# Kernel tuning notes

Measured on AMD Instinct MI355X. Metric: run time of the kernel, lower is better.

Reference implementation:

```python
import jax, jax.numpy as jnp
import numpy as np

ALPHA = 0.2  # LeakyReLU negative slope


def _gat_layer(x, edge_src, edge_dst, edge_embed, a, a2, concat):
    # torch: edge_h = cat(input[edge[0]], input[edge[1]], edge_embed).t(); scatter rows = edge[0]
    h = jnp.concatenate([x[edge_src], x[edge_dst], edge_embed], axis=1)  # [E, 2F+R]
    edge_m = h @ a.T                                                      # [E, D]
    powers = -jax.nn.leaky_relu(edge_m @ a2, ALPHA)                       # [E]
    edge_e = jnp.exp(powers)                                              # [E]
    N = x.shape[0]
    rowsum = jax.ops.segment_sum(edge_e, edge_src, num_segments=N)        # [N]
    rowsum = jnp.where(rowsum == 0.0, 1e-12, rowsum)
    h_prime = jax.ops.segment_sum(edge_e[:, None] * edge_m, edge_src, num_segments=N)  # [N, D]
    h_prime = h_prime / rowsum[:, None]
    return jax.nn.elu(h_prime) if concat else h_prime


def _spgat_forward(entity_embeddings, relation_embed, edge_embed, a, a2, W,
                   a_out, a2_out, edge_list, edge_type, edge_list_nhop, edge_type_nhop):
    nheads = a.shape[0]
    # concatenate 1-hop and n-hop edges (as in torch forward of the attention layer)
    src = jnp.concatenate([edge_list[0], edge_list_nhop[0]], axis=0)
    dst = jnp.concatenate([edge_list[1], edge_list_nhop[1]], axis=0)
    ee_nhop = relation_embed[edge_type_nhop[:, 0]] + relation_embed[edge_type_nhop[:, 1]]
    ee_all = jnp.concatenate([edge_embed, ee_nhop], axis=0)               # [E+E2, R]
    heads = [_gat_layer(entity_embeddings, src, dst, ee_all, a[i], a2[i], True)
             for i in range(nheads)]
    x = jnp.concatenate(heads, axis=1)                                    # [N, H*F] (dropout = identity, eval)
    out_relation_1 = relation_embed @ W                                   # [n_rel, H*F]
    ee2 = out_relation_1[edge_type]
    ee2_nhop = out_relation_1[edge_type_nhop[:, 0]] + out_relation_1[edge_type_nhop[:, 1]]
    ee2_all = jnp.concatenate([ee2, ee2_nhop], axis=0)                    # [E+E2, H*F]
    x = jax.nn.elu(_gat_layer(x, src, dst, ee2_all, a_out, a2_out, False))
    return x, out_relation_1


def setup_inputs() -> dict:
    key = jax.random.key(0)
    N, F, R, NREL, E, E2, H = 50000, 128, 128, 500, 150000, 30000, 2
    ks = jax.random.split(key, 12)

    def xavier(k, shape):
        fan_in, fan_out = shape[-1], shape[-2]
        std = 1.414 * np.sqrt(2.0 / (fan_in + fan_out))
        return (jax.random.normal(k, shape, dtype=jnp.float32) * std).astype(jnp.float32)

    return {
        "entity_embeddings": jax.random.normal(ks[0], (N, F), dtype=jnp.float32),
        "relation_embed": jax.random.normal(ks[1], (NREL, R), dtype=jnp.float32),
        "edge_embed": jax.random.normal(ks[2], (E, R), dtype=jnp.float32),
        "edge_list": jax.random.randint(ks[3], (2, E), 0, N),
        "edge_type": jax.random.randint(ks[4], (E,), 0, NREL),
        "edge_list_nhop": jax.random.randint(ks[5], (2, E2), 0, N),
        "edge_type_nhop": jax.random.randint(ks[6], (E2, 2), 0, NREL),
        "a": xavier(ks[7], (H, F, 2 * F + R)),            # per-head a: [D, 2F+R]
        "a2": xavier(ks[8], (H, 1, F))[:, 0, :],          # per-head a_2: [D]
        "W": xavier(ks[9], (R, H * F)),
        "a_out": xavier(ks[10], (H * F, 3 * H * F)),      # out layer: in=H*F, nrela=H*F
        "a2_out": xavier(ks[11], (1, H * F))[0],
    }


def reference(entity_embeddings, relation_embed, edge_embed, edge_list, edge_type,
              edge_list_nhop, edge_type_nhop, a, a2, W, a_out, a2_out):
    return _spgat_forward(entity_embeddings, relation_embed, edge_embed, a, a2, W,
                          a_out, a2_out, edge_list, edge_type, edge_list_nhop, edge_type_nhop)
```

## Files before the change

### kernel.cpp

```cpp
#include <hip/hip_runtime.h>
#include <cstdint>
#include <cstddef>

#define N_NODES 50000
#define MP1     50048
#define NRELC   500
#define E1      150000
#define MP2     150016
#define E2N     30000
#define ETOT    180000
#define ALPHA_F 0.2f

typedef __attribute__((ext_vector_type(8))) short bf16x8;
typedef __attribute__((ext_vector_type(4))) float f32x4;

__device__ __forceinline__ float bf2f(unsigned short s) {
  return __uint_as_float((unsigned)s << 16);
}
__device__ __forceinline__ unsigned short f2bf(float f) {
  unsigned u = __float_as_uint(f);
  u += 0x7fff + ((u >> 16) & 1);
  return (unsigned short)(u >> 16);
}

__global__ void zero_int(int* __restrict__ p, int n) {
  int i = blockIdx.x * blockDim.x + threadIdx.x;
  if (i < n) p[i] = 0;
}

__global__ void build_edges(const int* __restrict__ el, const int* __restrict__ elnh,
                            int* __restrict__ src, int* __restrict__ dst) {
  int e = blockIdx.x * blockDim.x + threadIdx.x;
  if (e >= ETOT) return;
  if (e < E1) { src[e] = el[e];        dst[e] = el[E1 + e]; }
  else        { int k = e - E1; src[e] = elnh[k]; dst[e] = elnh[E2N + k]; }
}

__global__ void count_edges(const int* __restrict__ src, int* __restrict__ cnt) {
  int e = blockIdx.x * blockDim.x + threadIdx.x;
  if (e < ETOT) atomicAdd(&cnt[src[e]], 1);
}

__global__ void scan_counts(const int* __restrict__ cnt, int* __restrict__ rowptr) {
  __shared__ int lds[1024];
  __shared__ int carry;
  if (threadIdx.x == 0) carry = 0;
  __syncthreads();
  for (int base = 0; base < N_NODES; base += 1024) {
    int i = base + (int)threadIdx.x;
    int v = (i < N_NODES) ? cnt[i] : 0;
    lds[threadIdx.x] = v;
    __syncthreads();
    for (int off = 1; off < 1024; off <<= 1) {
      int t = (threadIdx.x >= (unsigned)off) ? lds[threadIdx.x - off] : 0;
      __syncthreads();
      lds[threadIdx.x] += t;
      __syncthreads();
    }
    int incl = lds[threadIdx.x];
    if (i < N_NODES) rowptr[i] = carry + incl - v;
    __syncthreads();
    if (threadIdx.x == 1023) carry += lds[1023];
    __syncthreads();
  }
  if (threadIdx.x == 0) rowptr[N_NODES] = carry;
}

__global__ void copy_int(const int* __restrict__ a, int* __restrict__ b, int n) {
  int i = blockIdx.x * blockDim.x + threadIdx.x;
  if (i < n) b[i] = a[i];
}

__global__ void fill_csr(const int* __restrict__ src, int* __restrict__ pos, int* __restrict__ csr) {
  int e = blockIdx.x * blockDim.x + threadIdx.x;
  if (e >= ETOT) return;
  int p = atomicAdd(&pos[src[e]], 1);
  csr[p] = e;
}

__global__ void pack_weea3(const float* __restrict__ a, float* __restrict__ o) {
  int i = blockIdx.x * blockDim.x + threadIdx.x;
  if (i >= 256 * 128) return;
  int c = i >> 7, k = i & 127;
  int h = c >> 7, d = c & 127;
  o[i] = a[h * 49152 + d * 384 + 256 + k];
}
__global__ void pack_wtw(const float* __restrict__ w, float* __restrict__ o) {
  int i = blockIdx.x * blockDim.x + threadIdx.x;
  if (i >= 256 * 128) return;
  int n = i >> 7, k = i & 127;
  o[i] = w[k * 256 + n];
}
__global__ void pack_wa3out(const float* __restrict__ ao, float* __restrict__ o) {
  int i = blockIdx.x * blockDim.x + threadIdx.x;
  if (i >= 256 * 256) return;
  int d = i >> 8, k = i & 255;
  o[i] = ao[d * 768 + 512 + k];
}
__global__ void pack_wxa_bf(const float* __restrict__ a, unsigned short* __restrict__ o) {
  int i = blockIdx.x * blockDim.x + threadIdx.x;
  if (i >= 512 * 128) return;
  int c = i >> 7, k = i & 127;
  int h = c >> 8, part = (c >> 7) & 1, d = c & 127;
  o[i] = f2bf(a[h * 49152 + d * 384 + part * 128 + k]);
}
__global__ void pack_weea3_bf(const float* __restrict__ a, unsigned short* __restrict__ o) {
  int i = blockIdx.x * blockDim.x + threadIdx.x;
  if (i >= 256 * 128) return;
  int c = i >> 7, k = i & 127;
  int h = c >> 7, d = c & 127;
  o[i] = f2bf(a[h * 49152 + d * 384 + 256 + k]);
}
__global__ void pack_wx1a_bf(const float* __restrict__ ao, unsigned short* __restrict__ o) {
  int i = blockIdx.x * blockDim.x + threadIdx.x;
  if (i >= 512 * 256) return;
  int c = i >> 8, k = i & 255;
  int part = c >> 8, d = c & 255;
  o[i] = f2bf(ao[d * 768 + part * 256 + k]);
}

__global__ __launch_bounds__(256) void gemm_bt_f32(
    const float* __restrict__ A, const float* __restrict__ Wt,
    float* __restrict__ C, int M, int N, int K) {
  __shared__ float As[32][132];
  __shared__ float Bs[32][132];
  const int bm = blockIdx.x * 128;
  const int bn = blockIdx.y * 128;
  const int tid = threadIdx.x;
  const int tx = tid & 15;
  const int ty = tid >> 4;
  float acc[8][8];
#pragma unroll
  for (int i = 0; i < 8; ++i)
#pragma unroll
    for (int j = 0; j < 8; ++j) acc[i][j] = 0.f;

  const int lr = tid >> 3;
  const int lc = (tid & 7) << 2;

  for (int k0 = 0; k0 < K; k0 += 32) {
#pragma unroll
    for (int i = 0; i < 4; ++i) {
      const int row = lr + (i << 5);
      float4 av = make_float4(0.f, 0.f, 0.f, 0.f);
      float4 bv = make_float4(0.f, 0.f, 0.f, 0.f);
      const int ga = bm + row, gb = bn + row;
      if (ga < M) av = *reinterpret_cast<const float4*>(A + (size_t)ga * K + k0 + lc);
      if (gb < N) bv = *reinterpret_cast<const float4*>(Wt + (size_t)gb * K + k0 + lc);
      As[lc + 0][row] = av.x; As[lc + 1][row] = av.y; As[lc + 2][row] = av.z; As[lc + 3][row] = av.w;
      Bs[lc + 0][row] = bv.x; Bs[lc + 1][row] = bv.y; Bs[lc + 2][row] = bv.z; Bs[lc + 3][row] = bv.w;
    }
    __syncthreads();
    for (int kk = 0; kk < 32; ++kk) {
      float a8[8], b8[8];
      *(float4*)&a8[0] = *(const float4*)&As[kk][ty * 8];
      *(float4*)&a8[4] = *(const float4*)&As[kk][ty * 8 + 4];
      *(float4*)&b8[0] = *(const float4*)&Bs[kk][tx * 8];
      *(float4*)&b8[4] = *(const float4*)&Bs[kk][tx * 8 + 4];
#pragma unroll
      for (int i = 0; i < 8; ++i)
#pragma unroll
        for (int j = 0; j < 8; ++j) acc[i][j] = fmaf(a8[i], b8[j], acc[i][j]);
    }
    __syncthreads();
  }
#pragma unroll
  for (int i = 0; i < 8; ++i) {
    const int gr = bm + ty * 8 + i;
    if (gr < M) {
      float4 v0 = make_float4(acc[i][0], acc[i][1], acc[i][2], acc[i][3]);
      float4 v1 = make_float4(acc[i][4], acc[i][5], acc[i][6], acc[i][7]);
      *reinterpret_cast<float4*>(C + (size_t)gr * N + bn + tx * 8) = v0;
      *reinterpret_cast<float4*>(C + (size_t)gr * N + bn + tx * 8 + 4) = v1;
    }
  }
}

template <typename TA, int K>
__global__ __launch_bounds__(256) void gemm_mfma(
    const TA* __restrict__ A, const unsigned short* __restrict__ Wt,
    unsigned short* __restrict__ C, int Mreal, int N) {
  __shared__ __align__(16) unsigned short lds[2][8192];
  const int tid  = threadIdx.x;
  const int wave = tid >> 6;
  const int lane = tid & 63;
  const int bm = blockIdx.x * 128;
  const int bn = blockIdx.y * 128;
  const int wr = wave >> 1, wc = wave & 1;
  constexpr int NT = K / 32;

  f32x4 acc[4][4] = {};

  const int rb   = lane & 15;
  const int cofs = ((lane >> 4) ^ (lane & 3)) << 3;

  auto stageB = [&](int buf, int kt) {
#pragma unroll
    for (int j = 0; j < 2; ++j) {
      const int o   = (wave * 2 + j) * 1024 + lane * 16;
      const int row = o >> 6;
      const int sc  = (o & 63) ^ ((row & 3) << 4);
      const char* g = (const char*)Wt + (size_t)(bn + row) * (K * 2) + kt * 64 + sc;
      __builtin_amdgcn_global_load_lds(
          (const __attribute__((address_space(1))) void*)g,
          (__attribute__((address_space(3))) void*)&lds[buf][4096 + (wave * 2 + j) * 512],
          16, 0, 0);
    }
  };
  auto stageA = [&](int buf, int kt) {
    if constexpr (sizeof(TA) == 2) {
#pragma unroll
      for (int j = 0; j < 2; ++j) {
        const int o   = (wave * 2 + j) * 1024 + lane * 16;
        const int row = o >> 6;
        const int sc  = (o & 63) ^ ((row & 3) << 4);
        const char* g = (const char*)A + (size_t)(bm + row) * (K * 2) + kt * 64 + sc;
        __builtin_amdgcn_global_load_lds(
            (const __attribute__((address_space(1))) void*)g,
            (__attribute__((address_space(3))) void*)&lds[buf][(wave * 2 + j) * 512],
            16, 0, 0);
      }
    } else {
#pragma unroll
      for (int p = 0; p < 2; ++p) {
        const int o   = p * 4096 + tid * 16;
        const int row = o >> 6;
        const int ke  = ((o & 63) ^ ((row & 3) << 4)) >> 1;
        const int gr  = bm + row;
        float v[8];
#pragma unroll
        for (int q = 0; q < 8; ++q) v[q] = 0.f;
        if (gr < Mreal) {
          const float* gp = (const float*)A + (size_t)gr * K + kt * 32 + ke;
          float4 u0 = *(const float4*)gp;
          float4 u1 = *(const float4*)(gp + 4);
          v[0] = u0.x; v[1] = u0.y; v[2] = u0.z; v[3] = u0.w;
          v[4] = u1.x; v[5] = u1.y; v[6] = u1.z; v[7] = u1.w;
        }
        bf16x8 pk;
#pragma unroll
        for (int q = 0; q < 8; ++q) pk[q] = (short)f2bf(v[q]);
        *(bf16x8*)&lds[buf][o >> 1] = pk;
      }
    }
  };

  stageA(0, 0); stageB(0, 0);
  for (int t = 0; t < NT; ++t) {
    __syncthreads();
    if (t + 1 < NT) { stageA((t + 1) & 1, t + 1); stageB((t + 1) & 1, t + 1); }
    const int buf = t & 1;
    bf16x8 af[4], bfr[4];
#pragma unroll
    for (int m = 0; m < 4; ++m)
      af[m] = *(const bf16x8*)&lds[buf][(rb + 16 * m + 64 * wr) * 32 + cofs];
#pragma unroll
    for (int n = 0; n < 4; ++n)
      bfr[n] = *(const bf16x8*)&lds[buf][4096 + (rb + 16 * n + 64 * wc) * 32 + cofs];
#pragma unroll
    for (int m = 0; m < 4; ++m)
#pragma unroll
      for (int n = 0; n < 4; ++n)
        acc[m][n] = __builtin_amdgcn_mfma_f32_16x16x32_bf16(af[m], bfr[n], acc[m][n], 0, 0, 0);
  }

  const int ccol = bn + wc * 64 + rb;
  const int crow = bm + wr * 64 + ((lane >> 4) << 2);
#pragma unroll
  for (int m = 0; m < 4; ++m)
#pragma unroll
    for (int n = 0; n < 4; ++n)
#pragma unroll
      for (int r = 0; r < 4; ++r)
        C[(size_t)(crow + 16 * m + r) * N + ccol + 16 * n] = f2bf(acc[m][n][r]);
}

__global__ __launch_bounds__(256) void agg1(
    const unsigned short* __restrict__ xa, const unsigned short* __restrict__ eeA31,
    const float* __restrict__ relA3, const int* __restrict__ rowptr,
    const int* __restrict__ csr, const int* __restrict__ dst,
    const int* __restrict__ etnh, const float* __restrict__ a2,
    unsigned short* __restrict__ x1) {
  int w = blockIdx.x * 4 + (threadIdx.x >> 6);
  int n = w >> 1, h = w & 1;
  if (n >= N_NODES) return;
  int l = threadIdx.x & 63;
  float w2a = a2[h * 128 + l];
  float w2b = a2[h * 128 + 64 + l];
  const unsigned short* xan = xa + (size_t)n * 512 + h * 256;
  float s0 = bf2f(xan[l]), s1 = bf2f(xan[64 + l]);
  float acc0 = 0.f, acc1 = 0.f, rs = 0.f;
  int p0 = rowptr[n], p1 = rowptr[n + 1];
  for (int p = p0; p < p1; ++p) {
    int e = csr[p];
    int d = dst[e];
    const unsigned short* xad = xa + (size_t)d * 512 + h * 256 + 128;
    float m0 = s0 + bf2f(xad[l]);
    float m1 = s1 + bf2f(xad[64 + l]);
    if (e < E1) {
      const unsigned short* ee = eeA31 + (size_t)e * 256 + h * 128;
      m0 += bf2f(ee[l]); m1 += bf2f(ee[64 + l]);
    } else {
      int k = e - E1;
      int t0 = etnh[2 * k], t1 = etnh[2 * k + 1];
      const float* r0 = relA3 + t0 * 256 + h * 128;
      const float* r1 = relA3 + t1 * 256 + h * 128;
      m0 += r0[l] + r1[l];
      m1 += r0[64 + l] + r1[64 + l];
    }
    float dot = m0 * w2a + m1 * w2b;
#pragma unroll
    for (int off = 32; off; off >>= 1) dot += __shfl_xor(dot, off);
    float lk = dot > 0.f ? dot : ALPHA_F * dot;
    float ev = __expf(-lk);
    acc0 = fmaf(ev, m0, acc0);
    acc1 = fmaf(ev, m1, acc1);
    rs += ev;
  }
  if (rs == 0.f) rs = 1e-12f;
  float inv = 1.f / rs;
  float h0 = acc0 * inv, h1 = acc1 * inv;
  h0 = h0 > 0.f ? h0 : (__expf(h0) - 1.f);
  h1 = h1 > 0.f ? h1 : (__expf(h1) - 1.f);
  x1[(size_t)n * 256 + h * 128 + l] = f2bf(h0);
  x1[(size_t)n * 256 + h * 128 + 64 + l] = f2bf(h1);
}

__global__ __launch_bounds__(256) void agg2(
    const unsigned short* __restrict__ x1a, const float* __restrict__ rel2,
    const int* __restrict__ rowptr, const int* __restrict__ csr,
    const int* __restrict__ dst, const int* __restrict__ etype,
    const int* __restrict__ etnh, const float* __restrict__ a2o,
    float* __restrict__ out) {
  int n = blockIdx.x * 4 + (threadIdx.x >> 6);
  if (n >= N_NODES) return;
  int l = threadIdx.x & 63;
  float w2[4], s[4], acc[4] = {0.f, 0.f, 0.f, 0.f};
#pragma unroll
  for (int j = 0; j < 4; ++j) {
    w2[j] = a2o[j * 64 + l];
    s[j] = bf2f(x1a[(size_t)n * 512 + j * 64 + l]);
  }
  float rs = 0.f;
  int p0 = rowptr[n], p1 = rowptr[n + 1];
  for (int p = p0; p < p1; ++p) {
    int e = csr[p];
    int d = dst[e];
    const unsigned short* xd = x1a + (size_t)d * 512 + 256;
    float m[4];
    if (e < E1) {
      int t = etype[e];
      const float* r = rel2 + t * 256;
#pragma unroll
      for (int j = 0; j < 4; ++j) m[j] = s[j] + bf2f(xd[j * 64 + l]) + r[j * 64 + l];
    } else {
      int k = e - E1;
      int t0 = etnh[2 * k], t1 = etnh[2 * k + 1];
      const float* r0 = rel2 + t0 * 256;
      const float* r1 = rel2 + t1 * 256;
#pragma unroll
      for (int j = 0; j < 4; ++j) m[j] = s[j] + bf2f(xd[j * 64 + l]) + r0[j * 64 + l] + r1[j * 64 + l];
    }
    float dot = 0.f;
#pragma unroll
    for (int j = 0; j < 4; ++j) dot = fmaf(m[j], w2[j], dot);
#pragma unroll
    for (int off = 32; off; off >>= 1) dot += __shfl_xor(dot, off);
    float lk = dot > 0.f ? dot : ALPHA_F * dot;
    float ev = __expf(-lk);
#pragma unroll
    for (int j = 0; j < 4; ++j) acc[j] = fmaf(ev, m[j], acc[j]);
    rs += ev;
  }
  if (rs == 0.f) rs = 1e-12f;
  float inv = 1.f / rs;
#pragma unroll
  for (int j = 0; j < 4; ++j) {
    float hv = acc[j] * inv;
    hv = hv > 0.f ? hv : (__expf(hv) - 1.f);
    out[(size_t)n * 256 + j * 64 + l] = hv;
  }
}

extern "C" void kernel_launch(void* const* d_in, const int* in_sizes, int n_in,
                              void* d_out, int out_size, void* d_ws, size_t ws_size,
                              hipStream_t stream) {
  const float* x    = (const float*)d_in[0];
  const float* rel  = (const float*)d_in[1];
  const float* eemb = (const float*)d_in[2];
  const int*   el   = (const int*)d_in[3];
  const int*   et   = (const int*)d_in[4];
  const int*   elnh = (const int*)d_in[5];
  const int*   etnh = (const int*)d_in[6];
  const float* a    = (const float*)d_in[7];
  const float* a2   = (const float*)d_in[8];
  const float* W    = (const float*)d_in[9];
  const float* aout = (const float*)d_in[10];
  const float* a2o  = (const float*)d_in[11];

  char* ws = (char*)d_ws;
  size_t cur = 0;
  auto alloc = [&](size_t bytes) {
    size_t o = cur;
    cur = (cur + bytes + 511) & ~(size_t)511;
    return o;
  };
  int* src     = (int*)(ws + alloc((size_t)ETOT * 4));
  int* dstv    = (int*)(ws + alloc((size_t)ETOT * 4));
  int* rowptr  = (int*)(ws + alloc((size_t)(N_NODES + 1) * 4));
  int* pos     = (int*)(ws + alloc((size_t)N_NODES * 4));
  int* csr     = (int*)(ws + alloc((size_t)ETOT * 4));
  float* weea3f = (float*)(ws + alloc((size_t)256 * 128 * 4));
  float* wtw    = (float*)(ws + alloc((size_t)256 * 128 * 4));
  float* wa3o   = (float*)(ws + alloc((size_t)256 * 256 * 4));
  unsigned short* wxa_bf   = (unsigned short*)(ws + alloc((size_t)512 * 128 * 2));
  unsigned short* weea3_bf = (unsigned short*)(ws + alloc((size_t)256 * 128 * 2));
  unsigned short* wx1a_bf  = (unsigned short*)(ws + alloc((size_t)512 * 256 * 2));
  float* relA3 = (float*)(ws + alloc((size_t)NRELC * 256 * 4));
  float* rel2  = (float*)(ws + alloc((size_t)NRELC * 256 * 4));
  unsigned short* x1B = (unsigned short*)(ws + alloc((size_t)MP1 * 256 * 2));
  unsigned short* xaB = (unsigned short*)(ws + alloc((size_t)MP1 * 512 * 2));
  unsigned short* eeB = (unsigned short*)(ws + alloc((size_t)MP2 * 256 * 2));
  (void)ws_size; (void)in_sizes; (void)n_in; (void)out_size;

  float* out_x    = (float*)d_out;
  float* out_rel1 = out_x + (size_t)N_NODES * 256;

  zero_int<<<(N_NODES + 255) / 256, 256, 0, stream>>>(pos, N_NODES);
  build_edges<<<(ETOT + 255) / 256, 256, 0, stream>>>(el, elnh, src, dstv);
  count_edges<<<(ETOT + 255) / 256, 256, 0, stream>>>(src, pos);
  scan_counts<<<1, 1024, 0, stream>>>(pos, rowptr);
  copy_int<<<(N_NODES + 255) / 256, 256, 0, stream>>>(rowptr, pos, N_NODES);
  fill_csr<<<(ETOT + 255) / 256, 256, 0, stream>>>(src, pos, csr);

  pack_weea3<<<(256 * 128 + 255) / 256, 256, 0, stream>>>(a, weea3f);
  pack_wtw<<<(256 * 128 + 255) / 256, 256, 0, stream>>>(W, wtw);
  pack_wa3out<<<(256 * 256 + 255) / 256, 256, 0, stream>>>(aout, wa3o);
  pack_wxa_bf<<<(512 * 128 + 255) / 256, 256, 0, stream>>>(a, wxa_bf);
  pack_weea3_bf<<<(256 * 128 + 255) / 256, 256, 0, stream>>>(a, weea3_bf);
  pack_wx1a_bf<<<(512 * 256 + 255) / 256, 256, 0, stream>>>(aout, wx1a_bf);

  gemm_mfma<float, 128><<<dim3(MP1 / 128, 4), 256, 0, stream>>>(x, wxa_bf, xaB, N_NODES, 512);
  gemm_mfma<float, 128><<<dim3(MP2 / 128, 2), 256, 0, stream>>>(eemb, weea3_bf, eeB, E1, 256);
  gemm_bt_f32<<<dim3((NRELC + 127) / 128, 2), 256, 0, stream>>>(rel, weea3f, relA3, NRELC, 256, 128);

  agg1<<<(N_NODES * 2 + 3) / 4, 256, 0, stream>>>(xaB, eeB, relA3, rowptr, csr, dstv, etnh, a2, x1B);

  gemm_bt_f32<<<dim3((NRELC + 127) / 128, 2), 256, 0, stream>>>(rel, wtw, out_rel1, NRELC, 256, 128);
  gemm_bt_f32<<<dim3((NRELC + 127) / 128, 2), 256, 0, stream>>>(out_rel1, wa3o, rel2, NRELC, 256, 256);

  gemm_mfma<unsigned short, 256><<<dim3(MP1 / 128, 4), 256, 0, stream>>>(x1B, wx1a_bf, xaB, MP1, 512);

  agg2<<<(N_NODES + 3) / 4, 256, 0, stream>>>(xaB, rel2, rowptr, csr, dstv, et, etnh, a2o, out_x);
}
```

Before: 611.9 us.

## Replace single-block CSR scan with multi-block scan and fuse setup kernels

Swaps the serial single-block 1024-thread LDS scan over 50k node counts for a three-stage multi-block scan: wave-shuffle block scans, a scan of the block sums, and an add-offsets pass that also fills pos. Edge building is fused with counting, and the six weight-packing kernels become one launch. The aim is to cut a long serial kernel plus several launch overheads in the CSR build preamble. It adds two small extra launches and a branchy packing kernel.

```diff
diff --git a/kernel.cpp b/kernel.cpp
--- a/kernel.cpp
+++ b/kernel.cpp
@@ -10,6 +10,7 @@
 #define E2N     30000
 #define ETOT    180000
 #define ALPHA_F 0.2f
+#define NBSCAN  49
 
 typedef __attribute__((ext_vector_type(8))) short bf16x8;
 typedef __attribute__((ext_vector_type(4))) float f32x4;
@@ -28,47 +29,77 @@
   if (i < n) p[i] = 0;
 }
 
-__global__ void build_edges(const int* __restrict__ el, const int* __restrict__ elnh,
-                            int* __restrict__ src, int* __restrict__ dst) {
+__global__ void build_count(const int* __restrict__ el, const int* __restrict__ elnh,
+                            int* __restrict__ src, int* __restrict__ dst,
+                            int* __restrict__ cnt) {
   int e = blockIdx.x * blockDim.x + threadIdx.x;
   if (e >= ETOT) return;
-  if (e < E1) { src[e] = el[e];        dst[e] = el[E1 + e]; }
-  else        { int k = e - E1; src[e] = elnh[k]; dst[e] = elnh[E2N + k]; }
-}
-
-__global__ void count_edges(const int* __restrict__ src, int* __restrict__ cnt) {
-  int e = blockIdx.x * blockDim.x + threadIdx.x;
-  if (e < ETOT) atomicAdd(&cnt[src[e]], 1);
-}
-
-__global__ void scan_counts(const int* __restrict__ cnt, int* __restrict__ rowptr) {
-  __shared__ int lds[1024];
-  __shared__ int carry;
-  if (threadIdx.x == 0) carry = 0;
+  int s, d;
+  if (e < E1) { s = el[e];  d = el[E1 + e]; }
+  else        { int k = e - E1; s = elnh[k]; d = elnh[E2N + k]; }
+  src[e] = s; dst[e] = d;
+  atomicAdd(&cnt[s], 1);
+}
+
+__global__ __launch_bounds__(256) void block_scan(const int* __restrict__ cnt,
+                                                  int* __restrict__ rowptr,
+                                                  int* __restrict__ blocksum) {
+  __shared__ int wsum[4];
+  const int tid  = threadIdx.x;
+  const int lane = tid & 63;
+  const int wave = tid >> 6;
+  const int idx  = blockIdx.x * 1024 + tid * 4;
+  int v0 = 0, v1 = 0, v2 = 0, v3 = 0;
+  if (idx + 3 < N_NODES) {
+    int4 t = *reinterpret_cast<const int4*>(cnt + idx);
+    v0 = t.x; v1 = t.y; v2 = t.z; v3 = t.w;
+  } else {
+    if (idx + 0 < N_NODES) v0 = cnt[idx + 0];
+    if (idx + 1 < N_NODES) v1 = cnt[idx + 1];
+    if (idx + 2 < N_NODES) v2 = cnt[idx + 2];
+  }
+  const int tsum = v0 + v1 + v2 + v3;
+  int incl = tsum;
+#pragma unroll
+  for (int off = 1; off < 64; off <<= 1) {
+    int u = __shfl_up(incl, off);
+    if (lane >= off) incl += u;
+  }
+  if (lane == 63) wsum[wave] = incl;
   __syncthreads();
-  for (int base = 0; base < N_NODES; base += 1024) {
-    int i = base + (int)threadIdx.x;
-    int v = (i < N_NODES) ? cnt[i] : 0;
-    lds[threadIdx.x] = v;
-    __syncthreads();
-    for (int off = 1; off < 1024; off <<= 1) {
-      int t = (threadIdx.x >= (unsigned)off) ? lds[threadIdx.x - off] : 0;
-      __syncthreads();
-      lds[threadIdx.x] += t;
-      __syncthreads();
-    }
-    int incl = lds[threadIdx.x];
-    if (i < N_NODES) rowptr[i] = carry + incl - v;
-    __syncthreads();
-    if (threadIdx.x == 1023) carry += lds[1023];
-    __syncthreads();
-  }
-  if (threadIdx.x == 0) rowptr[N_NODES] = carry;
-}
-
-__global__ void copy_int(const int* __restrict__ a, int* __restrict__ b, int n) {
-  int i = blockIdx.x * blockDim.x + threadIdx.x;
-  if (i < n) b[i] = a[i];
+  int woff = 0;
+#pragma unroll
+  for (int w = 0; w < 4; ++w)
+    if (w < wave) woff += wsum[w];
+  const int ebase = woff + incl - tsum;
+  if (idx + 0 < N_NODES) rowptr[idx + 0] = ebase;
+  if (idx + 1 < N_NODES) rowptr[idx + 1] = ebase + v0;
+  if (idx + 2 < N_NODES) rowptr[idx + 2] = ebase + v0 + v1;
+  if (idx + 3 < N_NODES) rowptr[idx + 3] = ebase + v0 + v1 + v2;
+  if (tid == 255) blocksum[blockIdx.x] = woff + incl;
+}
+
+__global__ void scan_blocksums(int* __restrict__ blocksum, int* __restrict__ rowptr) {
+  const int lane = threadIdx.x & 63;
+  int v = (lane < NBSCAN) ? blocksum[lane] : 0;
+  int incl = v;
+#pragma unroll
+  for (int off = 1; off < 64; off <<= 1) {
+    int u = __shfl_up(incl, off);
+    if (lane >= off) incl += u;
+  }
+  if (lane < NBSCAN) blocksum[lane] = incl - v;
+  if (lane == 63) rowptr[N_NODES] = incl;
+}
+
+__global__ void add_offsets(int* __restrict__ rowptr, const int* __restrict__ blocksum,
+                            int* __restrict__ pos) {
+  int i = blockIdx.x * 256 + threadIdx.x;
+  if (i < N_NODES) {
+    int r = rowptr[i] + blocksum[i >> 10];
+    rowptr[i] = r;
+    pos[i] = r;
+  }
 }
 
 __global__ void fill_csr(const int* __restrict__ src, int* __restrict__ pos, int* __restrict__ csr) {
@@ -78,45 +109,44 @@
   csr[p] = e;
 }
 
-__global__ void pack_weea3(const float* __restrict__ a, float* __restrict__ o) {
+#define PK_TOT (32768 + 32768 + 65536 + 65536 + 32768 + 131072)
+__global__ void pack_all(const float* __restrict__ a, const float* __restrict__ W,
+                         const float* __restrict__ ao,
+                         float* __restrict__ weea3f, float* __restrict__ wtw,
+                         float* __restrict__ wa3o,
+                         unsigned short* __restrict__ wxa_bf,
+                         unsigned short* __restrict__ weea3_bf,
+                         unsigned short* __restrict__ wx1a_bf) {
   int i = blockIdx.x * blockDim.x + threadIdx.x;
-  if (i >= 256 * 128) return;
-  int c = i >> 7, k = i & 127;
-  int h = c >> 7, d = c & 127;
-  o[i] = a[h * 49152 + d * 384 + 256 + k];
-}
-__global__ void pack_wtw(const float* __restrict__ w, float* __restrict__ o) {
-  int i = blockIdx.x * blockDim.x + threadIdx.x;
-  if (i >= 256 * 128) return;
-  int n = i >> 7, k = i & 127;
-  o[i] = w[k * 256 + n];
-}
-__global__ void pack_wa3out(const float* __restrict__ ao, float* __restrict__ o) {
-  int i = blockIdx.x * blockDim.x + threadIdx.x;
-  if (i >= 256 * 256) return;
-  int d = i >> 8, k = i & 255;
-  o[i] = ao[d * 768 + 512 + k];
-}
-__global__ void pack_wxa_bf(const float* __restrict__ a, unsigned short* __restrict__ o) {
-  int i = blockIdx.x * blockDim.x + threadIdx.x;
-  if (i >= 512 * 128) return;
-  int c = i >> 7, k = i & 127;
-  int h = c >> 8, part = (c >> 7) & 1, d = c & 127;
-  o[i] = f2bf(a[h * 49152 + d * 384 + part * 128 + k]);
-}
-__global__ void pack_weea3_bf(const float* __restrict__ a, unsigned short* __restrict__ o) {
-  int i = blockIdx.x * blockDim.x + threadIdx.x;
-  if (i >= 256 * 128) return;
-  int c = i >> 7, k = i & 127;
-  int h = c >> 7, d = c & 127;
-  o[i] = f2bf(a[h * 49152 + d * 384 + 256 + k]);
-}
-__global__ void pack_wx1a_bf(const float* __restrict__ ao, unsigned short* __restrict__ o) {
-  int i = blockIdx.x * blockDim.x + threadIdx.x;
-  if (i >= 512 * 256) return;
-  int c = i >> 8, k = i & 255;
-  int part = c >> 8, d = c & 255;
-  o[i] = f2bf(ao[d * 768 + part * 256 + k]);
+  if (i >= PK_TOT) return;
+  if (i < 32768) {
+    int c = i >> 7, k = i & 127;
+    int h = c >> 7, d = c & 127;
+    weea3f[i] = a[h * 49152 + d * 384 + 256 + k];
+  } else if (i < 65536) {
+    int j = i - 32768;
+    int n = j >> 7, k = j & 127;
+    wtw[j] = W[k * 256 + n];
+  } else if (i < 131072) {
+    int j = i - 65536;
+    int d = j >> 8, k = j & 255;
+    wa3o[j] = ao[d * 768 + 512 + k];
+  } else if (i < 196608) {
+    int j = i - 131072;
+    int c = j >> 7, k = j & 127;
+    int h = c >> 8, part = (c >> 7) & 1, d = c & 127;
+    wxa_bf[j] = f2bf(a[h * 49152 + d * 384 + part * 128 + k]);
+  } else if (i < 229376) {
+    int j = i - 196608;
+    int c = j >> 7, k = j & 127;
+    int h = c >> 7, d = c & 127;
+    weea3_bf[j] = f2bf(a[h * 49152 + d * 384 + 256 + k]);
+  } else {
+    int j = i - 229376;
+    int c = j >> 8, k = j & 255;
+    int part = c >> 8, d = c & 255;
+    wx1a_bf[j] = f2bf(ao[d * 768 + part * 256 + k]);
+  }
 }
 
 __global__ __launch_bounds__(256) void gemm_bt_f32(
@@ -410,6 +440,7 @@
   int* rowptr  = (int*)(ws + alloc((size_t)(N_NODES + 1) * 4));
   int* pos     = (int*)(ws + alloc((size_t)N_NODES * 4));
   int* csr     = (int*)(ws + alloc((size_t)ETOT * 4));
+  int* bsum    = (int*)(ws + alloc((size_t)64 * 4));
   float* weea3f = (float*)(ws + alloc((size_t)256 * 128 * 4));
   float* wtw    = (float*)(ws + alloc((size_t)256 * 128 * 4));
   float* wa3o   = (float*)(ws + alloc((size_t)256 * 256 * 4));
@@ -427,18 +458,14 @@
   float* out_rel1 = out_x + (size_t)N_NODES * 256;
 
   zero_int<<<(N_NODES + 255) / 256, 256, 0, stream>>>(pos, N_NODES);
-  build_edges<<<(ETOT + 255) / 256, 256, 0, stream>>>(el, elnh, src, dstv);
-  count_edges<<<(ETOT + 255) / 256, 256, 0, stream>>>(src, pos);
-  scan_counts<<<1, 1024, 0, stream>>>(pos, rowptr);
-  copy_int<<<(N_NODES + 255) / 256, 256, 0, stream>>>(rowptr, pos, N_NODES);
+  build_count<<<(ETOT + 255) / 256, 256, 0, stream>>>(el, elnh, src, dstv, pos);
+  block_scan<<<NBSCAN, 256, 0, stream>>>(pos, rowptr, bsum);
+  scan_blocksums<<<1, 64, 0, stream>>>(bsum, rowptr);
+  add_offsets<<<(N_NODES + 255) / 256, 256, 0, stream>>>(rowptr, bsum, pos);
   fill_csr<<<(ETOT + 255) / 256, 256, 0, stream>>>(src, pos, csr);
 
-  pack_weea3<<<(256 * 128 + 255) / 256, 256, 0, stream>>>(a, weea3f);
-  pack_wtw<<<(256 * 128 + 255) / 256, 256, 0, stream>>>(W, wtw);
-  pack_wa3out<<<(256 * 256 + 255) / 256, 256, 0, stream>>>(aout, wa3o);
-  pack_wxa_bf<<<(512 * 128 + 255) / 256, 256, 0, stream>>>(a, wxa_bf);
-  pack_weea3_bf<<<(256 * 128 + 255) / 256, 256, 0, stream>>>(a, weea3_bf);
-  pack_wx1a_bf<<<(512 * 256 + 255) / 256, 256, 0, stream>>>(aout, wx1a_bf);
+  pack_all<<<(PK_TOT + 255) / 256, 256, 0, stream>>>(a, W, aout, weea3f, wtw, wa3o,
+                                                     wxa_bf, weea3_bf, wx1a_bf);
 
   gemm_mfma<float, 128><<<dim3(MP1 / 128, 4), 256, 0, stream>>>(x, wxa_bf, xaB, N_NODES, 512);
   gemm_mfma<float, 128><<<dim3(MP2 / 128, 2), 256, 0, stream>>>(eemb, weea3_bf, eeB, E1, 256);
```

Result: faster. 496.4 us (-18.9%).
